# Kernel optimization log

Measured on AMD Instinct MI355X. Metric: run time of the kernel, lower is better.

## Reference

```python
import jax, jax.numpy as jnp
import numpy as np

H = 8
DK = 16  # 128 // 8
DM = 128


def setup_inputs() -> dict:
    key = jax.random.key(0)
    ks = jax.random.split(key, 12)
    B, S = 4, 2048
    inp = {
        "query": jax.random.normal(ks[0], (B, S, DM), dtype=jnp.float32),
        "key": jax.random.normal(ks[1], (B, S, DM), dtype=jnp.float32),
        "value": jax.random.normal(ks[2], (B, S, DM), dtype=jnp.float32),
        "pos_embed": jax.random.normal(ks[3], (B, S, DM), dtype=jnp.float32),
        # three projection linears (shared: L0 for pos_query & query, L1 for pos_key & key, L2 for value)
        "W0": jax.random.normal(ks[4], (DM, DM), dtype=jnp.float32) / np.sqrt(DM),
        "b0": jnp.zeros((DM,), dtype=jnp.float32),
        "W1": jax.random.normal(ks[5], (DM, DM), dtype=jnp.float32) / np.sqrt(DM),
        "b1": jnp.zeros((DM,), dtype=jnp.float32),
        "W2": jax.random.normal(ks[6], (DM, DM), dtype=jnp.float32) / np.sqrt(DM),
        "b2": jnp.zeros((DM,), dtype=jnp.float32),
        "Wo": jax.random.normal(ks[7], (DM, DM), dtype=jnp.float32) / np.sqrt(DM),
        "bo": jnp.zeros((DM,), dtype=jnp.float32),
    }
    return inp


def _proj(x, W, b):
    # Linear then split heads: [B,S,128] -> [B,H,S,DK]
    B = x.shape[0]
    y = x @ W.T + b
    return y.reshape(B, -1, H, DK).transpose(0, 2, 1, 3)


def reference(query, key, value, pos_embed, W0, b0, W1, b1, W2, b2, Wo, bo):
    B = query.shape[0]
    pos1 = pos_embed[..., 0:DM]
    pos_q = _proj(pos1, W0, b0)  # shares L0 with query proj (as in source zip bug)
    pos_k = _proj(pos1, W1, b1)
    pos_attn = jnp.einsum("bhqd,bhkd->bhqk", pos_q, pos_k)  # [B,H,S,S]

    q = _proj(query, W0, b0)
    k = _proj(key, W1, b1)
    v = _proj(value, W2, b2)

    scale = 1.0 / jnp.sqrt(jnp.asarray(DK, dtype=q.dtype))
    scores = jnp.einsum("bhqd,bhkd->bhqk", q, k) * scale + pos_attn
    attn = jax.nn.softmax(scores, axis=-1)  # dropout = identity (eval)
    x = jnp.einsum("bhqk,bhkd->bhqd", attn, v)  # [B,H,S,DK]
    x = x.transpose(0, 2, 1, 3).reshape(B, -1, H * DK)
    return x @ Wo.T + bo
```

## Files before the change

kernel.cpp:

```cpp
#include <hip/hip_runtime.h>
#include <math.h>

#define LOG2E 1.44269504088896340736f

typedef __attribute__((ext_vector_type(8))) short bfrag;
typedef __attribute__((ext_vector_type(4))) float f4;
typedef unsigned __attribute__((ext_vector_type(2))) u2;

__device__ __forceinline__ unsigned pk_trunc(float a, float b) {
#if __has_builtin(__builtin_amdgcn_perm)
    return __builtin_amdgcn_perm(__float_as_uint(b), __float_as_uint(a), 0x07060302u);
#else
    return (__float_as_uint(a) >> 16) | (__float_as_uint(b) & 0xFFFF0000u);
#endif
}
__device__ __forceinline__ unsigned pk_rne(float a, float b) {
    unsigned ua = __float_as_uint(a); ua += 0x7FFFu + ((ua >> 16) & 1u);
    unsigned ub = __float_as_uint(b); ub += 0x7FFFu + ((ub >> 16) & 1u);
    return (ua >> 16) | (ub & 0xFFFF0000u);
}
__device__ __forceinline__ float trunchi(float x) {
    return __uint_as_float(__float_as_uint(x) & 0xFFFF0000u);
}
__device__ __forceinline__ float fexp2(float x) {
#if __has_builtin(__builtin_amdgcn_exp2f)
    return __builtin_amdgcn_exp2f(x);
#else
    return exp2f(x);
#endif
}
__device__ __forceinline__ void stage16(void* lds_base, const void* g) {
#if __has_builtin(__builtin_amdgcn_global_load_lds)
    __builtin_amdgcn_global_load_lds(
        (const __attribute__((address_space(1))) unsigned int*)g,
        (__attribute__((address_space(3))) unsigned int*)lds_base, 16, 0, 0);
#else
    int lane = threadIdx.x & 63;
    *(float4*)((char*)lds_base + lane * 16) = *(const float4*)g;
#endif
}
__device__ __forceinline__ f4 mfma_bf16(bfrag a, bfrag b, f4 c) {
    return __builtin_amdgcn_mfma_f32_16x16x32_bf16(a, b, c, 0, 0, 0);
}
__device__ __forceinline__ void conv8(const float* __restrict__ g, bfrag& hi, bfrag& lo) {
    f4 a = *(const f4*)g;
    f4 b = *(const f4*)(g + 4);
    union { unsigned u[4]; bfrag v; } H, L;
    H.u[0] = pk_trunc(a.x, a.y); H.u[1] = pk_trunc(a.z, a.w);
    H.u[2] = pk_trunc(b.x, b.y); H.u[3] = pk_trunc(b.z, b.w);
    L.u[0] = pk_trunc(a.x - trunchi(a.x), a.y - trunchi(a.y));
    L.u[1] = pk_trunc(a.z - trunchi(a.z), a.w - trunchi(a.w));
    L.u[2] = pk_trunc(b.x - trunchi(b.x), b.y - trunchi(b.y));
    L.u[3] = pk_trunc(b.z - trunchi(b.z), b.w - trunchi(b.w));
    hi = H.v; lo = L.v;
}
__device__ __forceinline__ void store_q2(f4 ea, f4 eb, char* base, int lodelta, int lane) {
    union { unsigned u[4]; bfrag v; } H, L;
    H.u[0] = pk_trunc(ea[0], ea[1]); H.u[1] = pk_trunc(ea[2], ea[3]);
    H.u[2] = pk_trunc(eb[0], eb[1]); H.u[3] = pk_trunc(eb[2], eb[3]);
    L.u[0] = pk_trunc(ea[0] - trunchi(ea[0]), ea[1] - trunchi(ea[1]));
    L.u[1] = pk_trunc(ea[2] - trunchi(ea[2]), ea[3] - trunchi(ea[3]));
    L.u[2] = pk_trunc(eb[0] - trunchi(eb[0]), eb[1] - trunchi(eb[1]));
    L.u[3] = pk_trunc(eb[2] - trunchi(eb[2]), eb[3] - trunchi(eb[3]));
    *(bfrag*)(base + lane * 16) = H.v;
    *(bfrag*)(base + lodelta + lane * 16) = L.v;
}
__device__ __forceinline__ void store_rne2(f4 ea, f4 eb, char* base, int lane) {
    union { unsigned u[4]; bfrag v; } P;
    P.u[0] = pk_rne(ea[0], ea[1]); P.u[1] = pk_rne(ea[2], ea[3]);
    P.u[2] = pk_rne(eb[0], eb[1]); P.u[3] = pk_rne(eb[2], eb[3]);
    *(bfrag*)(base + lane * 16) = P.v;
}

#define WS_QB 0u
#define WS_KV 8388608u
#define WS_XP 14680064u
#define WS_L  23068672u
#define WS_WI 23592960u

__global__ __launch_bounds__(256) void w_prep(
    const float* __restrict__ W0, const float* __restrict__ W1,
    const float* __restrict__ W2, const float* __restrict__ Wo,
    char* __restrict__ wimg)
{
    int wid = blockIdx.x * 4 + (threadIdx.x >> 6);
    int lane = threadIdx.x & 63;
    int img = wid >> 5, rem = wid & 31, tile = rem >> 2, kg = rem & 3;
    const float* W = (img <= 1) ? W0 : (img == 2) ? W1 : (img == 3) ? W2 : Wo;
    float s = (img == 0) ? 0.25f * LOG2E : (img == 1) ? LOG2E : 1.0f;
    int n = lane & 15, qd = lane >> 4;
    const float* rowp = W + (size_t)(tile * 16 + n) * 128 + kg * 32;
    f4 a, b;
    if (img == 4) { a = *(const f4*)(rowp + qd * 4); b = *(const f4*)(rowp + 16 + qd * 4); }
    else          { a = *(const f4*)(rowp + qd * 8); b = *(const f4*)(rowp + qd * 8 + 4); }
    a.x *= s; a.y *= s; a.z *= s; a.w *= s;
    b.x *= s; b.y *= s; b.z *= s; b.w *= s;
    union { unsigned u[4]; bfrag v; } H, L;
    H.u[0] = pk_trunc(a.x, a.y); H.u[1] = pk_trunc(a.z, a.w);
    H.u[2] = pk_trunc(b.x, b.y); H.u[3] = pk_trunc(b.z, b.w);
    L.u[0] = pk_trunc(a.x - trunchi(a.x), a.y - trunchi(a.y));
    L.u[1] = pk_trunc(a.z - trunchi(a.z), a.w - trunchi(a.w));
    L.u[2] = pk_trunc(b.x - trunchi(b.x), b.y - trunchi(b.y));
    L.u[3] = pk_trunc(b.z - trunchi(b.z), b.w - trunchi(b.w));
    char* dst = wimg + img * 65536 + tile * 8192 + kg * 2048;
    *(bfrag*)(dst + lane * 16) = H.v;
    *(bfrag*)(dst + 1024 + lane * 16) = L.v;
}

__global__ __launch_bounds__(256) void k_proj(
    const float* __restrict__ query, const float* __restrict__ key,
    const float* __restrict__ value, const float* __restrict__ pos,
    const float* __restrict__ b0, const float* __restrict__ b1,
    const float* __restrict__ b2,
    const char* __restrict__ wimg, char* __restrict__ qb, char* __restrict__ kv)
{
    __shared__ __align__(16) char xlds[65536];
    const int tid = threadIdx.x;
    const int bid = blockIdx.x;
    const int b = bid >> 6, s32 = bid & 63;
    const size_t rowbase = (size_t)(b * 2048 + s32 * 32);

#pragma unroll
    for (int i = 0; i < 8; ++i) {
        int cid = tid + i * 256;
        int arr = cid >> 9, rem = cid & 511;
        int c32 = rem >> 4, u = rem & 15;
        const float* sp = (arr == 0) ? query : (arr == 1) ? key
                        : (arr == 2) ? value : pos;
        bfrag hi, lo;
        conv8(sp + (rowbase + c32) * 128 + u * 8, hi, lo);
        int base = arr * 16384 + (c32 >> 4) * 8192 + (u >> 2) * 2048
                 + ((u & 3) * 16 + (c32 & 15)) * 16;
        *(bfrag*)(xlds + base) = hi;
        *(bfrag*)(xlds + base + 1024) = lo;
    }
    __syncthreads();

    const int w = tid >> 6, lane = tid & 63;
    const int n = lane & 15, qd = lane >> 4;
    const int h = blockIdx.y * 4 + w;
    const int bh = b * 8 + h;
    {
        bfrag wqh[4], wql[4], wph[4], wpl[4];
#pragma unroll
        for (int kg = 0; kg < 4; ++kg) {
            const char* wb = wimg + 0 * 65536 + h * 8192 + kg * 2048;
            wqh[kg] = *(const bfrag*)(wb + lane * 16);
            wql[kg] = *(const bfrag*)(wb + 1024 + lane * 16);
            const char* pb = wimg + 1 * 65536 + h * 8192 + kg * 2048;
            wph[kg] = *(const bfrag*)(pb + lane * 16);
            wpl[kg] = *(const bfrag*)(pb + 1024 + lane * 16);
        }
        float bq[4], bp[4];
#pragma unroll
        for (int r = 0; r < 4; ++r) {
            float bv = b0[h * 16 + qd * 4 + r];
            bq[r] = 0.25f * LOG2E * bv; bp[r] = LOG2E * bv;
        }
#pragma unroll
        for (int pp = 0; pp < 2; ++pp) {
            f4 cq = {bq[0], bq[1], bq[2], bq[3]};
            f4 cp = {bp[0], bp[1], bp[2], bp[3]};
#pragma unroll
            for (int kg = 0; kg < 4; ++kg) {
                const char* xq = xlds + 0 * 16384 + pp * 8192 + kg * 2048 + lane * 16;
                const char* xp_ = xlds + 3 * 16384 + pp * 8192 + kg * 2048 + lane * 16;
                bfrag xh = *(const bfrag*)xq, xl = *(const bfrag*)(xq + 1024);
                bfrag ph = *(const bfrag*)xp_, pl = *(const bfrag*)(xp_ + 1024);
                cq = mfma_bf16(wqh[kg], xh, cq);
                cq = mfma_bf16(wqh[kg], xl, cq);
                cq = mfma_bf16(wql[kg], xh, cq);
                cp = mfma_bf16(wph[kg], ph, cp);
                cp = mfma_bf16(wph[kg], pl, cp);
                cp = mfma_bf16(wpl[kg], ph, cp);
            }
            int pg = s32 * 2 + pp;
            store_q2(cq, cp, qb + (size_t)bh * 262144 + (size_t)pg * 2048, 1024, lane);
        }
    }
    {
        bfrag w1h[4], w1l[4];
#pragma unroll
        for (int kg = 0; kg < 4; ++kg) {
            const char* wb = wimg + 2 * 65536 + h * 8192 + kg * 2048;
            w1h[kg] = *(const bfrag*)(wb + lane * 16);
            w1l[kg] = *(const bfrag*)(wb + 1024 + lane * 16);
        }
        float bk[4];
#pragma unroll
        for (int r = 0; r < 4; ++r) bk[r] = b1[h * 16 + qd * 4 + r];
#pragma unroll
        for (int pp = 0; pp < 2; ++pp) {
            f4 ck = {bk[0], bk[1], bk[2], bk[3]};
            f4 cpk = {bk[0], bk[1], bk[2], bk[3]};
#pragma unroll
            for (int kg = 0; kg < 4; ++kg) {
                const char* xk = xlds + 1 * 16384 + pp * 8192 + kg * 2048 + lane * 16;
                const char* xp_ = xlds + 3 * 16384 + pp * 8192 + kg * 2048 + lane * 16;
                bfrag xh = *(const bfrag*)xk, xl = *(const bfrag*)(xk + 1024);
                bfrag ph = *(const bfrag*)xp_, pl = *(const bfrag*)(xp_ + 1024);
                ck = mfma_bf16(w1h[kg], xh, ck);
                ck = mfma_bf16(w1h[kg], xl, ck);
                ck = mfma_bf16(w1l[kg], xh, ck);
                cpk = mfma_bf16(w1h[kg], ph, cpk);
                cpk = mfma_bf16(w1h[kg], pl, cpk);
                cpk = mfma_bf16(w1l[kg], ph, cpk);
            }
            int pg = s32 * 2 + pp;
            store_rne2(ck, cpk,
                       kv + (size_t)bh * 196608 + (size_t)(pg >> 2) * 6144
                       + (pg & 3) * 1024, lane);
        }
    }
    {
        bfrag w2h[4], w2l[4];
#pragma unroll
        for (int kg = 0; kg < 4; ++kg) {
            const char* wb = wimg + 3 * 65536 + h * 8192 + kg * 2048;
            w2h[kg] = *(const bfrag*)(wb + lane * 16);
            w2l[kg] = *(const bfrag*)(wb + 1024 + lane * 16);
        }
        float bv = b2[h * 16 + n];
        f4 ca = {bv, bv, bv, bv};
        f4 cb = {bv, bv, bv, bv};
#pragma unroll
        for (int pp = 0; pp < 2; ++pp) {
#pragma unroll
            for (int kg = 0; kg < 4; ++kg) {
                const char* xv = xlds + 2 * 16384 + pp * 8192 + kg * 2048 + lane * 16;
                bfrag ah = *(const bfrag*)xv, al = *(const bfrag*)(xv + 1024);
                if (pp == 0) {
                    ca = mfma_bf16(ah, w2h[kg], ca);
                    ca = mfma_bf16(al, w2h[kg], ca);
                    ca = mfma_bf16(ah, w2l[kg], ca);
                } else {
                    cb = mfma_bf16(ah, w2h[kg], cb);
                    cb = mfma_bf16(al, w2h[kg], cb);
                    cb = mfma_bf16(ah, w2l[kg], cb);
                }
            }
        }
        store_rne2(ca, cb,
                   kv + (size_t)bh * 196608 + (size_t)(s32 >> 1) * 6144
                   + 4096 + (s32 & 1) * 1024, lane);
    }
}

__global__ __launch_bounds__(128, 4) void k_attn(
    const char* __restrict__ qb, const char* __restrict__ kvg,
    char* __restrict__ xp, float* __restrict__ lbuf)
{
    __shared__ __align__(16) char kbuf[2][6144];
    const int tid = threadIdx.x;
    const int w = tid >> 6, lane = tid & 63;
    const int bh = blockIdx.y, ks = blockIdx.z;
    const int q0 = blockIdx.x * 64 + w * 32;

    const char* qpb = qb + (size_t)bh * 262144 + (size_t)(q0 >> 4) * 2048;
    bfrag qh0 = *(const bfrag*)(qpb + lane * 16);
    bfrag ql0 = *(const bfrag*)(qpb + 1024 + lane * 16);
    bfrag qh1 = *(const bfrag*)(qpb + 2048 + lane * 16);
    bfrag ql1 = *(const bfrag*)(qpb + 3072 + lane * 16);

    const char* kvb = kvg + (size_t)bh * 196608 + (size_t)ks * 98304;

    union { unsigned u[4]; bfrag v; } onesu;
    onesu.u[0] = 0x3F803F80u; onesu.u[1] = 0x3F803F80u;
    onesu.u[2] = 0x3F803F80u; onesu.u[3] = 0x3F803F80u;
    const bfrag ones = onesu.v;

    f4 o0 = {0.f, 0.f, 0.f, 0.f}, o1 = {0.f, 0.f, 0.f, 0.f};
    f4 l0 = {0.f, 0.f, 0.f, 0.f}, l1 = {0.f, 0.f, 0.f, 0.f};

    auto stage = [&](char* db, const char* gsrc) {
#pragma unroll
        for (int i = 0; i < 3; ++i)
            stage16(db + (w * 3 + i) * 1024, gsrc + (w * 3 + i) * 1024 + lane * 16);
    };

    stage(kbuf[0], kvb);
    const char* gnext = kvb + 6144;
    int cur = 0;
    for (int ch = 0; ch < 16; ++ch) {
        asm volatile("s_waitcnt vmcnt(0)" ::: "memory");
        __syncthreads();
        if (ch < 15) { stage(kbuf[cur ^ 1], gnext); gnext += 6144; }
        const char* kb = kbuf[cur];
#pragma unroll
        for (int sub = 0; sub < 2; ++sub) {
            bfrag ka = *(const bfrag*)(kb + (2 * sub) * 1024 + lane * 16);
            bfrag kc2 = *(const bfrag*)(kb + (2 * sub + 1) * 1024 + lane * 16);
            bfrag vf = *(const bfrag*)(kb + 4096 + sub * 1024 + lane * 16);
            {
                f4 sa = {0.f, 0.f, 0.f, 0.f}, sb = {0.f, 0.f, 0.f, 0.f};
                sa = mfma_bf16(ka, qh0, sa);  sa = mfma_bf16(ka, ql0, sa);
                sb = mfma_bf16(kc2, qh0, sb); sb = mfma_bf16(kc2, ql0, sb);
                union { unsigned u[4]; bfrag v; } pf;
                pf.u[0] = pk_trunc(fexp2(sa[0]), fexp2(sa[1]));
                pf.u[1] = pk_trunc(fexp2(sa[2]), fexp2(sa[3]));
                pf.u[2] = pk_trunc(fexp2(sb[0]), fexp2(sb[1]));
                pf.u[3] = pk_trunc(fexp2(sb[2]), fexp2(sb[3]));
                o0 = mfma_bf16(vf, pf.v, o0);
                l0 = mfma_bf16(ones, pf.v, l0);
            }
            {
                f4 sa = {0.f, 0.f, 0.f, 0.f}, sb = {0.f, 0.f, 0.f, 0.f};
                sa = mfma_bf16(ka, qh1, sa);  sa = mfma_bf16(ka, ql1, sa);
                sb = mfma_bf16(kc2, qh1, sb); sb = mfma_bf16(kc2, ql1, sb);
                union { unsigned u[4]; bfrag v; } pf;
                pf.u[0] = pk_trunc(fexp2(sa[0]), fexp2(sa[1]));
                pf.u[1] = pk_trunc(fexp2(sa[2]), fexp2(sa[3]));
                pf.u[2] = pk_trunc(fexp2(sb[0]), fexp2(sb[1]));
                pf.u[3] = pk_trunc(fexp2(sb[2]), fexp2(sb[3]));
                o1 = mfma_bf16(vf, pf.v, o1);
                l1 = mfma_bf16(ones, pf.v, l1);
            }
        }
        cur ^= 1;
    }

    const int bbk = bh >> 3, h = bh & 7;
    const int gp0 = bbk * 128 + (q0 >> 4);
    char* xw = xp + (size_t)ks * 4194304 + (size_t)gp0 * 8192
             + (h >> 1) * 2048 + (h & 1) * 1024 + lane * 16;
    *(f4*)xw = o0;
    *(f4*)(xw + 8192) = o1;
    if (lane < 16) {
        float* lw = lbuf + (size_t)ks * 65536 + (size_t)bh * 2048 + q0 + lane;
        lw[0] = l0[0];
        lw[16] = l1[0];
    }
}

__global__ __launch_bounds__(128) void k_out(
    const char* __restrict__ xp, const float* __restrict__ lbuf,
    const char* __restrict__ wimg, const float* __restrict__ bo,
    float* __restrict__ out)
{
    const int tid = threadIdx.x;
    const int w = tid >> 6, lane = tid & 63;
    const int n = lane & 15, qd = lane >> 4;
    const int panel = blockIdx.x * 2 + w;
    const int row0 = panel * 16;
    const int rb = (panel & 127) * 16;
    const int b = panel >> 7;

    bfrag xf[4];
#pragma unroll
    for (int kg = 0; kg < 4; ++kg) {
        union { unsigned u[4]; bfrag v; } X;
#pragma unroll
        for (int half = 0; half < 2; ++half) {
            const char* pa = xp + (size_t)panel * 8192 + kg * 2048 + half * 1024 + lane * 16;
            f4 oa = *(const f4*)pa;
            f4 ob = *(const f4*)(pa + 4194304);
            int bh = b * 8 + kg * 2 + half;
            float la = lbuf[(size_t)bh * 2048 + rb + n];
            float lb = lbuf[65536 + (size_t)bh * 2048 + rb + n];
            float inv = 1.0f / (la + lb);
            float v0 = (oa[0] + ob[0]) * inv, v1 = (oa[1] + ob[1]) * inv;
            float v2 = (oa[2] + ob[2]) * inv, v3 = (oa[3] + ob[3]) * inv;
            X.u[half * 2] = pk_rne(v0, v1);
            X.u[half * 2 + 1] = pk_rne(v2, v3);
        }
        xf[kg] = X.v;
    }

#pragma unroll
    for (int t = 0; t < 8; ++t) {
        float bv = bo[t * 16 + n];
        f4 cacc = {bv, bv, bv, bv};
#pragma unroll
        for (int kg = 0; kg < 4; ++kg) {
            const char* wb = wimg + 4 * 65536 + t * 8192 + kg * 2048;
            bfrag wh = *(const bfrag*)(wb + lane * 16);
            bfrag wl = *(const bfrag*)(wb + 1024 + lane * 16);
            cacc = mfma_bf16(xf[kg], wh, cacc);
            cacc = mfma_bf16(xf[kg], wl, cacc);
        }
#pragma unroll
        for (int r = 0; r < 4; ++r)
            out[(size_t)(row0 + qd * 4 + r) * 128 + t * 16 + n] = cacc[r];
    }
}

extern "C" void kernel_launch(void* const* d_in, const int* in_sizes, int n_in,
                              void* d_out, int out_size, void* d_ws, size_t ws_size,
                              hipStream_t stream)
{
    const float* query = (const float*)d_in[0];
    const float* key   = (const float*)d_in[1];
    const float* value = (const float*)d_in[2];
    const float* pos   = (const float*)d_in[3];
    const float* W0 = (const float*)d_in[4];
    const float* b0 = (const float*)d_in[5];
    const float* W1 = (const float*)d_in[6];
    const float* b1 = (const float*)d_in[7];
    const float* W2 = (const float*)d_in[8];
    const float* b2 = (const float*)d_in[9];
    const float* Wo = (const float*)d_in[10];
    const float* bo = (const float*)d_in[11];

    char* ws = (char*)d_ws;
    char* qbuf = ws + WS_QB;
    char* kv   = ws + WS_KV;
    char* xp   = ws + WS_XP;
    float* lb  = (float*)(ws + WS_L);
    char* wimg = ws + WS_WI;
    float* out = (float*)d_out;

    w_prep<<<dim3(40), 256, 0, stream>>>(W0, W1, W2, Wo, wimg);
    k_proj<<<dim3(256, 2), 256, 0, stream>>>(query, key, value, pos, b0, b1, b2,
                                             wimg, qbuf, kv);
    k_attn<<<dim3(32, 32, 2), 128, 0, stream>>>(qbuf, kv, xp, lb);
    k_out<<<dim3(256), 128, 0, stream>>>(xp, lb, wimg, bo, out);
}
```

Measured before the change: 130.1 us.

## Fold weight bf16 split into projection and output kernels, drop w_prep launch

Removes the separate w_prep kernel and has k_proj and k_out read fp32 weights directly, scaling and splitting them into hi/lo bf16 fragments in registers. This saves one kernel launch and the workspace round trip for the weight image. k_out is also re-gridded to one wave per block with a 2D grid of 512x4, so each block computes only two output column tiles. The cost is redundant weight conversion in every block, and W0 is loaded twice per k_proj wave.

```diff
diff --git a/kernel.cpp b/kernel.cpp
--- a/kernel.cpp
+++ b/kernel.cpp
@@ -42,9 +42,7 @@
 __device__ __forceinline__ f4 mfma_bf16(bfrag a, bfrag b, f4 c) {
     return __builtin_amdgcn_mfma_f32_16x16x32_bf16(a, b, c, 0, 0, 0);
 }
-__device__ __forceinline__ void conv8(const float* __restrict__ g, bfrag& hi, bfrag& lo) {
-    f4 a = *(const f4*)g;
-    f4 b = *(const f4*)(g + 4);
+__device__ __forceinline__ void conv8v(f4 a, f4 b, bfrag& hi, bfrag& lo) {
     union { unsigned u[4]; bfrag v; } H, L;
     H.u[0] = pk_trunc(a.x, a.y); H.u[1] = pk_trunc(a.z, a.w);
     H.u[2] = pk_trunc(b.x, b.y); H.u[3] = pk_trunc(b.z, b.w);
@@ -53,6 +51,16 @@
     L.u[2] = pk_trunc(b.x - trunchi(b.x), b.y - trunchi(b.y));
     L.u[3] = pk_trunc(b.z - trunchi(b.z), b.w - trunchi(b.w));
     hi = H.v; lo = L.v;
+}
+__device__ __forceinline__ void conv8(const float* __restrict__ g, bfrag& hi, bfrag& lo) {
+    conv8v(*(const f4*)g, *(const f4*)(g + 4), hi, lo);
+}
+__device__ __forceinline__ void conv8s(const float* __restrict__ g, float s,
+                                       bfrag& hi, bfrag& lo) {
+    f4 a = *(const f4*)g, b = *(const f4*)(g + 4);
+    a.x *= s; a.y *= s; a.z *= s; a.w *= s;
+    b.x *= s; b.y *= s; b.z *= s; b.w *= s;
+    conv8v(a, b, hi, lo);
 }
 __device__ __forceinline__ void store_q2(f4 ea, f4 eb, char* base, int lodelta, int lane) {
     union { unsigned u[4]; bfrag v; } H, L;
@@ -76,43 +84,15 @@
 #define WS_KV 8388608u
 #define WS_XP 14680064u
 #define WS_L  23068672u
-#define WS_WI 23592960u
-
-__global__ __launch_bounds__(256) void w_prep(
-    const float* __restrict__ W0, const float* __restrict__ W1,
-    const float* __restrict__ W2, const float* __restrict__ Wo,
-    char* __restrict__ wimg)
-{
-    int wid = blockIdx.x * 4 + (threadIdx.x >> 6);
-    int lane = threadIdx.x & 63;
-    int img = wid >> 5, rem = wid & 31, tile = rem >> 2, kg = rem & 3;
-    const float* W = (img <= 1) ? W0 : (img == 2) ? W1 : (img == 3) ? W2 : Wo;
-    float s = (img == 0) ? 0.25f * LOG2E : (img == 1) ? LOG2E : 1.0f;
-    int n = lane & 15, qd = lane >> 4;
-    const float* rowp = W + (size_t)(tile * 16 + n) * 128 + kg * 32;
-    f4 a, b;
-    if (img == 4) { a = *(const f4*)(rowp + qd * 4); b = *(const f4*)(rowp + 16 + qd * 4); }
-    else          { a = *(const f4*)(rowp + qd * 8); b = *(const f4*)(rowp + qd * 8 + 4); }
-    a.x *= s; a.y *= s; a.z *= s; a.w *= s;
-    b.x *= s; b.y *= s; b.z *= s; b.w *= s;
-    union { unsigned u[4]; bfrag v; } H, L;
-    H.u[0] = pk_trunc(a.x, a.y); H.u[1] = pk_trunc(a.z, a.w);
-    H.u[2] = pk_trunc(b.x, b.y); H.u[3] = pk_trunc(b.z, b.w);
-    L.u[0] = pk_trunc(a.x - trunchi(a.x), a.y - trunchi(a.y));
-    L.u[1] = pk_trunc(a.z - trunchi(a.z), a.w - trunchi(a.w));
-    L.u[2] = pk_trunc(b.x - trunchi(b.x), b.y - trunchi(b.y));
-    L.u[3] = pk_trunc(b.z - trunchi(b.z), b.w - trunchi(b.w));
-    char* dst = wimg + img * 65536 + tile * 8192 + kg * 2048;
-    *(bfrag*)(dst + lane * 16) = H.v;
-    *(bfrag*)(dst + 1024 + lane * 16) = L.v;
-}
 
 __global__ __launch_bounds__(256) void k_proj(
     const float* __restrict__ query, const float* __restrict__ key,
     const float* __restrict__ value, const float* __restrict__ pos,
+    const float* __restrict__ W0, const float* __restrict__ W1,
+    const float* __restrict__ W2,
     const float* __restrict__ b0, const float* __restrict__ b1,
     const float* __restrict__ b2,
-    const char* __restrict__ wimg, char* __restrict__ qb, char* __restrict__ kv)
+    char* __restrict__ qb, char* __restrict__ kv)
 {
     __shared__ __align__(16) char xlds[65536];
     const int tid = threadIdx.x;
@@ -140,16 +120,14 @@
     const int n = lane & 15, qd = lane >> 4;
     const int h = blockIdx.y * 4 + w;
     const int bh = b * 8 + h;
+    const size_t wrow = (size_t)(h * 16 + n) * 128 + qd * 8;
+
     {
         bfrag wqh[4], wql[4], wph[4], wpl[4];
 #pragma unroll
         for (int kg = 0; kg < 4; ++kg) {
-            const char* wb = wimg + 0 * 65536 + h * 8192 + kg * 2048;
-            wqh[kg] = *(const bfrag*)(wb + lane * 16);
-            wql[kg] = *(const bfrag*)(wb + 1024 + lane * 16);
-            const char* pb = wimg + 1 * 65536 + h * 8192 + kg * 2048;
-            wph[kg] = *(const bfrag*)(pb + lane * 16);
-            wpl[kg] = *(const bfrag*)(pb + 1024 + lane * 16);
+            conv8s(W0 + wrow + kg * 32, 0.25f * LOG2E, wqh[kg], wql[kg]);
+            conv8s(W0 + wrow + kg * 32, LOG2E, wph[kg], wpl[kg]);
         }
         float bq[4], bp[4];
 #pragma unroll
@@ -181,11 +159,8 @@
     {
         bfrag w1h[4], w1l[4];
 #pragma unroll
-        for (int kg = 0; kg < 4; ++kg) {
-            const char* wb = wimg + 2 * 65536 + h * 8192 + kg * 2048;
-            w1h[kg] = *(const bfrag*)(wb + lane * 16);
-            w1l[kg] = *(const bfrag*)(wb + 1024 + lane * 16);
-        }
+        for (int kg = 0; kg < 4; ++kg)
+            conv8(W1 + wrow + kg * 32, w1h[kg], w1l[kg]);
         float bk[4];
 #pragma unroll
         for (int r = 0; r < 4; ++r) bk[r] = b1[h * 16 + qd * 4 + r];
@@ -215,11 +190,8 @@
     {
         bfrag w2h[4], w2l[4];
 #pragma unroll
-        for (int kg = 0; kg < 4; ++kg) {
-            const char* wb = wimg + 3 * 65536 + h * 8192 + kg * 2048;
-            w2h[kg] = *(const bfrag*)(wb + lane * 16);
-            w2l[kg] = *(const bfrag*)(wb + 1024 + lane * 16);
-        }
+        for (int kg = 0; kg < 4; ++kg)
+            conv8(W2 + wrow + kg * 32, w2h[kg], w2l[kg]);
         float bv = b2[h * 16 + n];
         f4 ca = {bv, bv, bv, bv};
         f4 cb = {bv, bv, bv, bv};
@@ -332,15 +304,14 @@
     }
 }
 
-__global__ __launch_bounds__(128) void k_out(
+__global__ __launch_bounds__(64) void k_out(
     const char* __restrict__ xp, const float* __restrict__ lbuf,
-    const char* __restrict__ wimg, const float* __restrict__ bo,
+    const float* __restrict__ Wo, const float* __restrict__ bo,
     float* __restrict__ out)
 {
-    const int tid = threadIdx.x;
-    const int w = tid >> 6, lane = tid & 63;
+    const int lane = threadIdx.x;
     const int n = lane & 15, qd = lane >> 4;
-    const int panel = blockIdx.x * 2 + w;
+    const int panel = blockIdx.x;
     const int row0 = panel * 16;
     const int rb = (panel & 127) * 16;
     const int b = panel >> 7;
@@ -367,14 +338,15 @@
     }
 
 #pragma unroll
-    for (int t = 0; t < 8; ++t) {
+    for (int tt = 0; tt < 2; ++tt) {
+        int t = blockIdx.y * 2 + tt;
         float bv = bo[t * 16 + n];
         f4 cacc = {bv, bv, bv, bv};
 #pragma unroll
         for (int kg = 0; kg < 4; ++kg) {
-            const char* wb = wimg + 4 * 65536 + t * 8192 + kg * 2048;
-            bfrag wh = *(const bfrag*)(wb + lane * 16);
-            bfrag wl = *(const bfrag*)(wb + 1024 + lane * 16);
+            const float* wr = Wo + (size_t)(t * 16 + n) * 128 + kg * 32;
+            bfrag wh, wl;
+            conv8v(*(const f4*)(wr + qd * 4), *(const f4*)(wr + 16 + qd * 4), wh, wl);
             cacc = mfma_bf16(xf[kg], wh, cacc);
             cacc = mfma_bf16(xf[kg], wl, cacc);
         }
@@ -406,12 +378,10 @@
     char* kv   = ws + WS_KV;
     char* xp   = ws + WS_XP;
     float* lb  = (float*)(ws + WS_L);
-    char* wimg = ws + WS_WI;
     float* out = (float*)d_out;
 
-    w_prep<<<dim3(40), 256, 0, stream>>>(W0, W1, W2, Wo, wimg);
-    k_proj<<<dim3(256, 2), 256, 0, stream>>>(query, key, value, pos, b0, b1, b2,
-                                             wimg, qbuf, kv);
+    k_proj<<<dim3(256, 2), 256, 0, stream>>>(query, key, value, pos,
+                                             W0, W1, W2, b0, b1, b2, qbuf, kv);
     k_attn<<<dim3(32, 32, 2), 128, 0, stream>>>(qbuf, kv, xp, lb);
-    k_out<<<dim3(256), 128, 0, stream>>>(xp, lb, wimg, bo, out);
-}
+    k_out<<<dim3(512, 4), 64, 0, stream>>>(xp, lb, Wo, bo, out);
+}
```

After: 126.9 us (median of 2 runs). 1.03x faster.
